# Performance work log

Measured on AMD Instinct MI355X. Metric: run time of the kernel, lower is better.

The kernel has to match this reference:

```python
import jax, jax.numpy as jnp
import numpy as np

B, S, D, H = 4, 2048, 1024, 16
HD = D // H

def setup_inputs() -> dict:
    key = jax.random.key(0)
    ks = jax.random.split(key, 10)
    s = 1.0 / np.sqrt(D)
    inp = {
        'x': jax.random.normal(ks[0], (B, S, D), dtype=jnp.float32),
        'attention_mask': jnp.ones((B, S), dtype=jnp.int32),
        'Wq': jax.random.uniform(ks[1], (D, D), jnp.float32, -s, s),
        'bq': jax.random.uniform(ks[2], (D,), jnp.float32, -s, s),
        'Wk': jax.random.uniform(ks[3], (D, D), jnp.float32, -s, s),
        'bk': jax.random.uniform(ks[4], (D,), jnp.float32, -s, s),
        'Wv': jax.random.uniform(ks[5], (D, D), jnp.float32, -s, s),
        'bv': jax.random.uniform(ks[6], (D,), jnp.float32, -s, s),
        'Wo': jax.random.uniform(ks[7], (D, D), jnp.float32, -s, s),
        'bo': jax.random.uniform(ks[8], (D,), jnp.float32, -s, s),
    }
    return inp

def reference(x, Wq, bq, Wk, bk, Wv, bv, Wo, bo, attention_mask):
    scale = HD ** -0.5
    # torch Linear: y = x @ W^T + b
    def proj(W, b):
        return (x @ W.T + b).reshape(B, S, H, HD).transpose(0, 2, 1, 3)  # [B,H,S,hd]
    q = proj(Wq, bq)
    k = proj(Wk, bk)
    v = proj(Wv, bv)
    scores = jnp.einsum('bhqd,bhkd->bhqk', q, k) * scale  # [B,H,S,S]
    causal = jnp.triu(jnp.ones((S, S), dtype=bool), k=1)
    scores = jnp.where(causal, -jnp.inf, scores)
    pad = (attention_mask == 0)[:, None, None, :]  # [B,1,1,S]
    scores = jnp.where(pad, jnp.float32(-1e9), scores)
    probs = jax.nn.softmax(scores, axis=-1)
    out = jnp.einsum('bhqk,bhkd->bhqd', probs, v)  # [B,H,S,hd]
    out = out.transpose(0, 2, 1, 3).reshape(B, S, D)
    return out @ Wo.T + bo
```

## Files before the change

kernel.cpp:

```cpp
#include <hip/hip_runtime.h>
#include <hip/hip_bf16.h>

typedef unsigned short u16;
typedef float f32x4 __attribute__((ext_vector_type(4)));
typedef __bf16 bf16x8 __attribute__((ext_vector_type(8)));

#define BB 4
#define SS 2048
#define DD 1024
#define HH 16
#define HDD 64
#define MM (BB*SS)

__device__ __forceinline__ u16 f2bf(float f){
    union { float f; unsigned int i; } v; v.f = f;
    unsigned int i = v.i;
    return (u16)((i + 0x7FFFu + ((i >> 16) & 1u)) >> 16);
}
__device__ __forceinline__ ushort2 pk2(float a, float b){
    union { __hip_bfloat162 h; ushort2 u; } v;
    float2 t; t.x = a; t.y = b;
    v.h = __float22bfloat162_rn(t);
    return v.u;
}
__device__ __forceinline__ ushort4 pk4(float a, float b, float c, float d){
    ushort2 lo = pk2(a, b), hi = pk2(c, d);
    ushort4 r; r.x = lo.x; r.y = lo.y; r.z = hi.x; r.w = hi.y;
    return r;
}
__device__ __forceinline__ void gl2lds16(const void* g, void* l){
    __builtin_amdgcn_global_load_lds(
        (const __attribute__((address_space(1))) void*)g,
        (__attribute__((address_space(3))) void*)l, 16, 0, 0);
}

__device__ __forceinline__ void cvt8(const float* __restrict__ src,
                                     u16* __restrict__ dst, size_t i)
{
    const float4 a = *(const float4*)&src[i];
    const float4 b = *(const float4*)&src[i + 4];
    ushort4 lo = pk4(a.x, a.y, a.z, a.w);
    ushort4 hi = pk4(b.x, b.y, b.z, b.w);
    uint4 o;
    o.x = (unsigned)lo.x | ((unsigned)lo.y << 16);
    o.y = (unsigned)lo.z | ((unsigned)lo.w << 16);
    o.z = (unsigned)hi.x | ((unsigned)hi.y << 16);
    o.w = (unsigned)hi.z | ((unsigned)hi.w << 16);
    *(uint4*)&dst[i] = o;
}

__global__ __launch_bounds__(256) void cvt_k(const float* __restrict__ src,
                                             u16* __restrict__ dst)
{
    const size_t i = ((size_t)blockIdx.x * 256 + threadIdx.x) * 8;
    cvt8(src, dst, i);
}

__global__ __launch_bounds__(256) void cvtw_k(
    const float* __restrict__ W0, const float* __restrict__ W1,
    const float* __restrict__ W2, const float* __restrict__ W3,
    u16* __restrict__ dst)
{
    const float* src = blockIdx.y == 0 ? W0 : (blockIdx.y == 1 ? W1 :
                        (blockIdx.y == 2 ? W2 : W3));
    u16* d = dst + (size_t)blockIdx.y * (size_t)DD * DD;
    const size_t i = ((size_t)blockIdx.x * 256 + threadIdx.x) * 8;
    cvt8(src, d, i);
}

template<bool WB>
__device__ __forceinline__ void gemm_core_t(const u16* __restrict__ A,
                                            const float* __restrict__ Wf,
                                            const u16* __restrict__ Wb,
                                            f32x4 (&acc)[4][4],
                                            u16* At, u16* Bt,
                                            int m0, int n0, int tid)
{
    const int lane = tid & 63, w = tid >> 6;
    const int quad = lane >> 4, l15 = lane & 15;
    const int wm = w >> 1, wn = w & 1;
    const int arow = lane >> 2;
    const int acol = (lane & 3) * 8;

    for (int k0 = 0; k0 < DD; k0 += 32) {
        __syncthreads();
        #pragma unroll
        for (int c = 0; c < 2; ++c) {
            const int ch = w * 2 + c;
            gl2lds16(&A[(size_t)(m0 + ch * 16 + arow) * DD + k0 + acol], &At[ch * 512]);
        }
        if (WB) {
            #pragma unroll
            for (int c = 0; c < 2; ++c) {
                const int ch = w * 2 + c;
                gl2lds16(&Wb[(size_t)(n0 + ch * 16 + arow) * DD + k0 + acol], &Bt[ch * 512]);
            }
        } else {
            #pragma unroll
            for (int it = 0; it < 2; ++it) {
                const int c = tid + it * 256;
                const int row = c >> 2, cc = (c & 3) * 8;
                const size_t woff = (size_t)(n0 + row) * DD + k0 + cc;
                const float4 u0 = *(const float4*)&Wf[woff];
                const float4 u1 = *(const float4*)&Wf[woff + 4];
                ushort4 lo = pk4(u0.x, u0.y, u0.z, u0.w);
                ushort4 hi = pk4(u1.x, u1.y, u1.z, u1.w);
                uint4 o;
                o.x = (unsigned)lo.x | ((unsigned)lo.y << 16);
                o.y = (unsigned)lo.z | ((unsigned)lo.w << 16);
                o.z = (unsigned)hi.x | ((unsigned)hi.y << 16);
                o.w = (unsigned)hi.z | ((unsigned)hi.w << 16);
                *(uint4*)&Bt[row * 32 + cc] = o;
            }
        }
        __syncthreads();
        bf16x8 af[4], bfr[4];
        #pragma unroll
        for (int i = 0; i < 4; ++i)
            af[i] = *(const bf16x8*)&At[(wm * 64 + i * 16 + l15) * 32 + quad * 8];
        #pragma unroll
        for (int j = 0; j < 4; ++j)
            bfr[j] = *(const bf16x8*)&Bt[(wn * 64 + j * 16 + l15) * 32 + quad * 8];
        #pragma unroll
        for (int i = 0; i < 4; ++i)
            #pragma unroll
            for (int j = 0; j < 4; ++j)
                acc[i][j] = __builtin_amdgcn_mfma_f32_16x16x32_bf16(af[i], bfr[j], acc[i][j], 0, 0, 0);
    }
}

template<bool WB>
__global__ __launch_bounds__(256, 4) void gemm_qkv_k(
    const u16* __restrict__ x,
    const float* __restrict__ Wq, const float* __restrict__ bq,
    const float* __restrict__ Wk, const float* __restrict__ bk,
    const float* __restrict__ Wv, const float* __restrict__ bv,
    const u16* __restrict__ Wqb, const u16* __restrict__ Wkb,
    const u16* __restrict__ Wvb,
    u16* __restrict__ Q, u16* __restrict__ K, u16* __restrict__ V)
{
    __shared__ alignas(16) u16 At[128 * 32];
    __shared__ alignas(16) u16 Bt[128 * 32];
    const int tid = threadIdx.x, lane = tid & 63, w = tid >> 6;
    const int quad = lane >> 4, l15 = lane & 15;
    const int wm = w >> 1, wn = w & 1;
    const int z = blockIdx.z;
    const float* Wm = z == 0 ? Wq : (z == 1 ? Wk : Wv);
    const u16* Wmb = z == 0 ? Wqb : (z == 1 ? Wkb : Wvb);
    const float* bias = z == 0 ? bq : (z == 1 ? bk : bv);
    u16* Out = z == 0 ? Q : (z == 1 ? K : V);
    const int m0 = blockIdx.x * 128, n0 = blockIdx.y * 128;

    f32x4 acc[4][4];
    #pragma unroll
    for (int i = 0; i < 4; ++i)
        #pragma unroll
        for (int j = 0; j < 4; ++j) acc[i][j] = (f32x4)(0.0f);

    gemm_core_t<WB>(x, Wm, Wmb, acc, At, Bt, m0, n0, tid);

    float bs[4];
    #pragma unroll
    for (int j = 0; j < 4; ++j) bs[j] = bias[n0 + wn * 64 + j * 16 + l15];

    const int b = m0 / SS;
    const int h = (n0 + wn * 64) / HDD;
    const size_t base = ((size_t)(b * HH + h)) * SS * HDD;
    #pragma unroll
    for (int i = 0; i < 4; ++i) {
        #pragma unroll
        for (int r = 0; r < 4; ++r) {
            const int s = (m0 % SS) + wm * 64 + i * 16 + quad * 4 + r;
            #pragma unroll
            for (int j = 0; j < 4; ++j) {
                const int hd = j * 16 + l15;
                Out[base + (size_t)s * HDD + hd] = f2bf(acc[i][j][r] + bs[j]);
            }
        }
    }
}

template<bool WB>
__global__ __launch_bounds__(256, 4) void gemm_out_k(
    const u16* __restrict__ A, const float* __restrict__ Wo,
    const float* __restrict__ bo, const u16* __restrict__ Wob,
    float* __restrict__ Out)
{
    __shared__ alignas(16) u16 At[128 * 32];
    __shared__ alignas(16) u16 Bt[128 * 32];
    const int tid = threadIdx.x, lane = tid & 63, w = tid >> 6;
    const int quad = lane >> 4, l15 = lane & 15;
    const int wm = w >> 1, wn = w & 1;
    const int m0 = blockIdx.x * 128, n0 = blockIdx.y * 128;

    f32x4 acc[4][4];
    #pragma unroll
    for (int i = 0; i < 4; ++i)
        #pragma unroll
        for (int j = 0; j < 4; ++j) acc[i][j] = (f32x4)(0.0f);

    gemm_core_t<WB>(A, Wo, Wob, acc, At, Bt, m0, n0, tid);

    float bs[4];
    #pragma unroll
    for (int j = 0; j < 4; ++j) bs[j] = bo[n0 + wn * 64 + j * 16 + l15];

    #pragma unroll
    for (int i = 0; i < 4; ++i) {
        #pragma unroll
        for (int r = 0; r < 4; ++r) {
            const int m = m0 + wm * 64 + i * 16 + quad * 4 + r;
            #pragma unroll
            for (int j = 0; j < 4; ++j) {
                const int n = n0 + wn * 64 + j * 16 + l15;
                Out[(size_t)m * DD + n] = acc[i][j][r] + bs[j];
            }
        }
    }
}

#define QT 256
#define KT 64
#define LDP 72
#define LDPV 66

#define LOG2E 1.4426950408889634f

__global__ __launch_bounds__(512, 2) void attn_k(
    const u16* __restrict__ Q, const u16* __restrict__ K,
    const u16* __restrict__ V, const int* __restrict__ mask,
    u16* __restrict__ AO)
{
    __shared__ alignas(16) u16 QPs[QT * LDP];
    __shared__ alignas(16) u16 Ks[2][KT * LDP];
    __shared__ alignas(16) u16 Vs[2][HDD * LDPV];
    __shared__ alignas(16) float padf[2][KT];

    const int tid = threadIdx.x, lane = tid & 63, w = tid >> 6;
    const int quad = lane >> 4, l15 = lane & 15;
    const int bh = blockIdx.x;
    const int y = blockIdx.y;
    const int qt = (y < 4) ? (7 - y) : (y - 4);
    const int b = bh >> 4, h = bh & 15;
    const int q0 = qt * QT;
    const size_t hoff = (size_t)bh * SS * HDD;
    const u16* Qh = Q + hoff;
    const u16* Kh = K + hoff;
    const u16* Vh = V + hoff;
    const int nkt = (q0 + QT) / KT;
    const float scale2 = 0.125f * LOG2E;

    uint4 kr0, kr1, vr0, vr1, vr2, vr3;
    float pr = 0.f;

    auto LOADT = [&](int kt0) {
        if (tid < 256) {
            const int row0 = tid >> 3, cc0 = (tid & 7) * 8;
            kr0 = *(const uint4*)&Kh[(size_t)(kt0 + row0) * HDD + cc0];
            const int row1 = (tid + 256) >> 3, cc1 = ((tid + 256) & 7) * 8;
            kr1 = *(const uint4*)&Kh[(size_t)(kt0 + row1) * HDD + cc1];
        } else if (tid < 384) {
            const int t = tid - 256;
            const int kq = t >> 3, c0 = (t & 7) * 8;
            vr0 = *(const uint4*)&Vh[(size_t)(kt0 + kq * 4 + 0) * HDD + c0];
            vr1 = *(const uint4*)&Vh[(size_t)(kt0 + kq * 4 + 1) * HDD + c0];
            vr2 = *(const uint4*)&Vh[(size_t)(kt0 + kq * 4 + 2) * HDD + c0];
            vr3 = *(const uint4*)&Vh[(size_t)(kt0 + kq * 4 + 3) * HDD + c0];
        } else if (tid < 448) {
            pr = (mask[b * SS + kt0 + (tid - 384)] == 0) ? -1e9f : 0.0f;
        }
    };
    auto WRITET = [&](int bb) {
        if (tid < 256) {
            const int row0 = tid >> 3, cc0 = (tid & 7) * 8;
            *(uint4*)&Ks[bb][row0 * LDP + cc0] = kr0;
            const int row1 = (tid + 256) >> 3, cc1 = ((tid + 256) & 7) * 8;
            *(uint4*)&Ks[bb][row1 * LDP + cc1] = kr1;
        } else if (tid < 384) {
            const int t = tid - 256;
            const int kq = t >> 3, c0 = (t & 7) * 8;
            const u16* e0 = (const u16*)&vr0;
            const u16* e1 = (const u16*)&vr1;
            const u16* e2 = (const u16*)&vr2;
            const u16* e3 = (const u16*)&vr3;
            #pragma unroll
            for (int e = 0; e < 8; ++e) {
                ushort4 pkv; pkv.x = e0[e]; pkv.y = e1[e]; pkv.z = e2[e]; pkv.w = e3[e];
                *(ushort4*)&Vs[bb][(c0 + e) * LDPV + kq * 4] = pkv;
            }
        } else if (tid < 448) {
            padf[bb][tid - 384] = pr;
        }
    };

    LOADT(0);

    for (int c = tid; c < QT * 8; c += 512) {
        const int row = c >> 3, cc = c & 7;
        *(uint4*)&QPs[row * LDP + cc * 8] = *(const uint4*)&Qh[(size_t)(q0 + row) * HDD + cc * 8];
    }
    WRITET(0);
    __syncthreads();

    bf16x8 bQ[2][2];
    #pragma unroll
    for (int j = 0; j < 2; ++j)
        #pragma unroll
        for (int ks = 0; ks < 2; ++ks)
            bQ[j][ks] = *(const bf16x8*)&QPs[(w * 32 + j * 16 + l15) * LDP + ks * 32 + quad * 8];

    float m_run[2] = { -1e30f, -1e30f };
    float l_run[2] = { 0.f, 0.f };
    f32x4 o[4][2];
    #pragma unroll
    for (int i = 0; i < 4; ++i)
        #pragma unroll
        for (int j = 0; j < 2; ++j) o[i][j] = (f32x4)(0.0f);

    for (int kt = 0; kt < nkt; ++kt) {
        const int cur = kt & 1;
        const int kt0 = kt * KT;
        if (kt + 1 < nkt) LOADT(kt0 + KT);

        const u16* KsC = Ks[cur];
        const u16* VsC = Vs[cur];
        const float* padfC = padf[cur];

        f32x4 sc[4][2];
        #pragma unroll
        for (int i = 0; i < 4; ++i)
            #pragma unroll
            for (int j = 0; j < 2; ++j) sc[i][j] = (f32x4)(0.0f);
        __builtin_amdgcn_s_setprio(1);
        #pragma unroll
        for (int ks = 0; ks < 2; ++ks) {
            bf16x8 aK[4];
            #pragma unroll
            for (int i = 0; i < 4; ++i)
                aK[i] = *(const bf16x8*)&KsC[(i * 16 + l15) * LDP + ks * 32 + quad * 8];
            #pragma unroll
            for (int i = 0; i < 4; ++i)
                #pragma unroll
                for (int j = 0; j < 2; ++j)
                    sc[i][j] = __builtin_amdgcn_mfma_f32_16x16x32_bf16(aK[i], bQ[j][ks], sc[i][j], 0, 0, 0);
        }
        __builtin_amdgcn_s_setprio(0);

        f32x4 pb[4];
        #pragma unroll
        for (int i = 0; i < 4; ++i)
            pb[i] = *(const f32x4*)&padfC[i * 16 + quad * 4];

        #pragma unroll
        for (int j = 0; j < 2; ++j) {
            const int qrow = q0 + w * 32 + j * 16 + l15;
            const bool needC = (kt0 + KT - 1) > (q0 + w * 32 + j * 16);
            float mx = -1e9f;
            if (needC) {
                #pragma unroll
                for (int i = 0; i < 4; ++i)
                    #pragma unroll
                    for (int r = 0; r < 4; ++r) {
                        const int kpg = kt0 + i * 16 + quad * 4 + r;
                        float s = fmaf(sc[i][j][r], scale2, pb[i][r]);
                        s = (kpg > qrow) ? -1e9f : s;
                        sc[i][j][r] = s; mx = fmaxf(mx, s);
                    }
            } else {
                #pragma unroll
                for (int i = 0; i < 4; ++i)
                    #pragma unroll
                    for (int r = 0; r < 4; ++r) {
                        float s = fmaf(sc[i][j][r], scale2, pb[i][r]);
                        sc[i][j][r] = s; mx = fmaxf(mx, s);
                    }
            }
            mx = fmaxf(mx, __shfl_xor(mx, 16, 64));
            mx = fmaxf(mx, __shfl_xor(mx, 32, 64));
            float nm = m_run[j];
            if (!__all(mx <= nm + 8.f)) {
                nm = fmaxf(nm, mx);
                const float alpha = __builtin_exp2f(m_run[j] - nm);
                m_run[j] = nm;
                l_run[j] *= alpha;
                #pragma unroll
                for (int i = 0; i < 4; ++i)
                    #pragma unroll
                    for (int r = 0; r < 4; ++r) o[i][j][r] *= alpha;
            }
            float rs = 0.f;
            #pragma unroll
            for (int i = 0; i < 4; ++i) {
                float p0 = __builtin_exp2f(sc[i][j][0] - nm);
                float p1 = __builtin_exp2f(sc[i][j][1] - nm);
                float p2 = __builtin_exp2f(sc[i][j][2] - nm);
                float p3 = __builtin_exp2f(sc[i][j][3] - nm);
                rs += (p0 + p1) + (p2 + p3);
                *(ushort4*)&QPs[(w * 32 + j * 16 + l15) * LDP + i * 16 + quad * 4] = pk4(p0, p1, p2, p3);
            }
            l_run[j] += rs;
        }
        asm volatile("s_waitcnt lgkmcnt(0)" ::: "memory");

        __builtin_amdgcn_s_setprio(1);
        #pragma unroll
        for (int ks = 0; ks < 2; ++ks) {
            bf16x8 aV[4], bP[2];
            #pragma unroll
            for (int i = 0; i < 4; ++i)
                aV[i] = *(const bf16x8*)&VsC[(i * 16 + l15) * LDPV + ks * 32 + quad * 8];
            #pragma unroll
            for (int j = 0; j < 2; ++j)
                bP[j] = *(const bf16x8*)&QPs[(w * 32 + j * 16 + l15) * LDP + ks * 32 + quad * 8];
            #pragma unroll
            for (int i = 0; i < 4; ++i)
                #pragma unroll
                for (int j = 0; j < 2; ++j)
                    o[i][j] = __builtin_amdgcn_mfma_f32_16x16x32_bf16(aV[i], bP[j], o[i][j], 0, 0, 0);
        }
        __builtin_amdgcn_s_setprio(0);

        if (kt + 1 < nkt) WRITET(cur ^ 1);
        __syncthreads();
    }

    #pragma unroll
    for (int j = 0; j < 2; ++j) {
        float l = l_run[j];
        l += __shfl_xor(l, 16, 64);
        l += __shfl_xor(l, 32, 64);
        const float inv = (l > 0.f) ? (1.f / l) : 0.f;
        const int s = q0 + w * 32 + j * 16 + l15;
        const size_t rb = ((size_t)(b * SS + s)) * DD + h * HDD;
        #pragma unroll
        for (int i = 0; i < 4; ++i)
            *(ushort4*)&AO[rb + i * 16 + quad * 4] =
                pk4(o[i][j][0] * inv, o[i][j][1] * inv, o[i][j][2] * inv, o[i][j][3] * inv);
    }
}

extern "C" void kernel_launch(void* const* d_in, const int* in_sizes, int n_in,
                              void* d_out, int out_size, void* d_ws, size_t ws_size,
                              hipStream_t stream)
{
    const float* x  = (const float*)d_in[0];
    const int* mask = (const int*)d_in[1];
    const float* Wq = (const float*)d_in[2];
    const float* bq = (const float*)d_in[3];
    const float* Wk = (const float*)d_in[4];
    const float* bk = (const float*)d_in[5];
    const float* Wv = (const float*)d_in[6];
    const float* bv = (const float*)d_in[7];
    const float* Wo = (const float*)d_in[8];
    const float* bo = (const float*)d_in[9];
    float* out = (float*)d_out;

    u16* ws = (u16*)d_ws;
    const size_t NE = (size_t)MM * DD;
    const size_t WE = (size_t)DD * DD;
    if (ws_size < 4 * NE * sizeof(u16)) return;
    const bool wb = ws_size >= (4 * NE + 4 * WE) * sizeof(u16);

    u16* Qb = ws;
    u16* Kb = ws + NE;
    u16* Vb = ws + 2 * NE;
    u16* Ab = ws + 3 * NE;

    dim3 blk(256);
    cvt_k<<<dim3(NE / 2048), blk, 0, stream>>>(x, Ab);
    if (wb) {
        u16* Wbase = ws + 4 * NE;
        cvtw_k<<<dim3(WE / 2048, 4), blk, 0, stream>>>(Wq, Wk, Wv, Wo, Wbase);
        gemm_qkv_k<true><<<dim3(MM / 128, DD / 128, 3), blk, 0, stream>>>(
            Ab, Wq, bq, Wk, bk, Wv, bv,
            Wbase, Wbase + WE, Wbase + 2 * WE, Qb, Kb, Vb);
        attn_k<<<dim3(BB * HH, SS / QT), dim3(512), 0, stream>>>(Qb, Kb, Vb, mask, Ab);
        gemm_out_k<true><<<dim3(MM / 128, DD / 128), blk, 0, stream>>>(
            Ab, Wo, bo, Wbase + 3 * WE, out);
    } else {
        gemm_qkv_k<false><<<dim3(MM / 128, DD / 128, 3), blk, 0, stream>>>(
            Ab, Wq, bq, Wk, bk, Wv, bv,
            nullptr, nullptr, nullptr, Qb, Kb, Vb);
        attn_k<<<dim3(BB * HH, SS / QT), dim3(512), 0, stream>>>(Qb, Kb, Vb, mask, Ab);
        gemm_out_k<false><<<dim3(MM / 128, DD / 128), blk, 0, stream>>>(
            Ab, Wo, bo, nullptr, out);
    }
}
```

Before: 359.9 us.

## Drop K/V double buffering, swizzle LDS, raise attention occupancy to 3 blocks

The attention kernel drops the register-staged double buffer for K, V and the pad mask and loads each tile directly into a single LDS buffer, with a barrier before and after each load. Q/P and K tiles switch from padded rows to an XOR-swizzled 128-byte row layout, which cuts LDS footprint and avoids bank conflicts. With less LDS and fewer live staging registers, launch bounds ask for 3 blocks per CU instead of 2. The trade-off is that global load latency is no longer overlapped within a block and must be hidden by the extra resident blocks, plus an added barrier per tile.

```diff
diff --git a/kernel.cpp b/kernel.cpp
--- a/kernel.cpp
+++ b/kernel.cpp
@@ -221,20 +221,23 @@
 
 #define QT 256
 #define KT 64
-#define LDP 72
 #define LDPV 66
 
 #define LOG2E 1.4426950408889634f
 
-__global__ __launch_bounds__(512, 2) void attn_k(
+__device__ __forceinline__ int swz128(int row, int bcol){
+    return row * 128 + (bcol ^ ((row & 7) << 4));
+}
+
+__global__ __launch_bounds__(512, 3) void attn_k(
     const u16* __restrict__ Q, const u16* __restrict__ K,
     const u16* __restrict__ V, const int* __restrict__ mask,
     u16* __restrict__ AO)
 {
-    __shared__ alignas(16) u16 QPs[QT * LDP];
-    __shared__ alignas(16) u16 Ks[2][KT * LDP];
-    __shared__ alignas(16) u16 Vs[2][HDD * LDPV];
-    __shared__ alignas(16) float padf[2][KT];
+    __shared__ alignas(16) u16 QPs[QT * 64];
+    __shared__ alignas(16) u16 Ks[KT * 64];
+    __shared__ alignas(16) u16 Vs[HDD * LDPV];
+    __shared__ float padf[KT];
 
     const int tid = threadIdx.x, lane = tid & 63, w = tid >> 6;
     const int quad = lane >> 4, l15 = lane & 15;
@@ -250,56 +253,11 @@
     const int nkt = (q0 + QT) / KT;
     const float scale2 = 0.125f * LOG2E;
 
-    uint4 kr0, kr1, vr0, vr1, vr2, vr3;
-    float pr = 0.f;
-
-    auto LOADT = [&](int kt0) {
-        if (tid < 256) {
-            const int row0 = tid >> 3, cc0 = (tid & 7) * 8;
-            kr0 = *(const uint4*)&Kh[(size_t)(kt0 + row0) * HDD + cc0];
-            const int row1 = (tid + 256) >> 3, cc1 = ((tid + 256) & 7) * 8;
-            kr1 = *(const uint4*)&Kh[(size_t)(kt0 + row1) * HDD + cc1];
-        } else if (tid < 384) {
-            const int t = tid - 256;
-            const int kq = t >> 3, c0 = (t & 7) * 8;
-            vr0 = *(const uint4*)&Vh[(size_t)(kt0 + kq * 4 + 0) * HDD + c0];
-            vr1 = *(const uint4*)&Vh[(size_t)(kt0 + kq * 4 + 1) * HDD + c0];
-            vr2 = *(const uint4*)&Vh[(size_t)(kt0 + kq * 4 + 2) * HDD + c0];
-            vr3 = *(const uint4*)&Vh[(size_t)(kt0 + kq * 4 + 3) * HDD + c0];
-        } else if (tid < 448) {
-            pr = (mask[b * SS + kt0 + (tid - 384)] == 0) ? -1e9f : 0.0f;
-        }
-    };
-    auto WRITET = [&](int bb) {
-        if (tid < 256) {
-            const int row0 = tid >> 3, cc0 = (tid & 7) * 8;
-            *(uint4*)&Ks[bb][row0 * LDP + cc0] = kr0;
-            const int row1 = (tid + 256) >> 3, cc1 = ((tid + 256) & 7) * 8;
-            *(uint4*)&Ks[bb][row1 * LDP + cc1] = kr1;
-        } else if (tid < 384) {
-            const int t = tid - 256;
-            const int kq = t >> 3, c0 = (t & 7) * 8;
-            const u16* e0 = (const u16*)&vr0;
-            const u16* e1 = (const u16*)&vr1;
-            const u16* e2 = (const u16*)&vr2;
-            const u16* e3 = (const u16*)&vr3;
-            #pragma unroll
-            for (int e = 0; e < 8; ++e) {
-                ushort4 pkv; pkv.x = e0[e]; pkv.y = e1[e]; pkv.z = e2[e]; pkv.w = e3[e];
-                *(ushort4*)&Vs[bb][(c0 + e) * LDPV + kq * 4] = pkv;
-            }
-        } else if (tid < 448) {
-            padf[bb][tid - 384] = pr;
-        }
-    };
-
-    LOADT(0);
-
     for (int c = tid; c < QT * 8; c += 512) {
         const int row = c >> 3, cc = c & 7;
-        *(uint4*)&QPs[row * LDP + cc * 8] = *(const uint4*)&Qh[(size_t)(q0 + row) * HDD + cc * 8];
-    }
-    WRITET(0);
+        *(uint4*)((char*)QPs + swz128(row, cc * 16)) =
+            *(const uint4*)&Qh[(size_t)(q0 + row) * HDD + cc * 8];
+    }
     __syncthreads();
 
     bf16x8 bQ[2][2];
@@ -307,7 +265,8 @@
     for (int j = 0; j < 2; ++j)
         #pragma unroll
         for (int ks = 0; ks < 2; ++ks)
-            bQ[j][ks] = *(const bf16x8*)&QPs[(w * 32 + j * 16 + l15) * LDP + ks * 32 + quad * 8];
+            bQ[j][ks] = *(const bf16x8*)((const char*)QPs +
+                swz128(w * 32 + j * 16 + l15, ks * 64 + quad * 16));
 
     float m_run[2] = { -1e30f, -1e30f };
     float l_run[2] = { 0.f, 0.f };
@@ -318,13 +277,39 @@
         for (int j = 0; j < 2; ++j) o[i][j] = (f32x4)(0.0f);
 
     for (int kt = 0; kt < nkt; ++kt) {
-        const int cur = kt & 1;
         const int kt0 = kt * KT;
-        if (kt + 1 < nkt) LOADT(kt0 + KT);
-
-        const u16* KsC = Ks[cur];
-        const u16* VsC = Vs[cur];
-        const float* padfC = padf[cur];
+        __syncthreads();
+
+        if (tid < 256) {
+            #pragma unroll
+            for (int it = 0; it < 2; ++it) {
+                const int c = tid + it * 256;
+                const int row = c >> 3, cc = c & 7;
+                *(uint4*)((char*)Ks + swz128(row, cc * 16)) =
+                    *(const uint4*)&Kh[(size_t)(kt0 + row) * HDD + cc * 8];
+            }
+        } else if (tid < 384) {
+            const int t = tid - 256;
+            const int kq = t >> 3;
+            const int c0 = (t & 7) * 8;
+            uint4 r0 = *(const uint4*)&Vh[(size_t)(kt0 + kq * 4 + 0) * HDD + c0];
+            uint4 r1 = *(const uint4*)&Vh[(size_t)(kt0 + kq * 4 + 1) * HDD + c0];
+            uint4 r2 = *(const uint4*)&Vh[(size_t)(kt0 + kq * 4 + 2) * HDD + c0];
+            uint4 r3 = *(const uint4*)&Vh[(size_t)(kt0 + kq * 4 + 3) * HDD + c0];
+            const u16* e0 = (const u16*)&r0;
+            const u16* e1 = (const u16*)&r1;
+            const u16* e2 = (const u16*)&r2;
+            const u16* e3 = (const u16*)&r3;
+            #pragma unroll
+            for (int e = 0; e < 8; ++e) {
+                ushort4 pkv; pkv.x = e0[e]; pkv.y = e1[e]; pkv.z = e2[e]; pkv.w = e3[e];
+                *(ushort4*)&Vs[(c0 + e) * LDPV + kq * 4] = pkv;
+            }
+        } else if (tid < 448) {
+            const int t = tid - 384;
+            padf[t] = (mask[b * SS + kt0 + t] == 0) ? -1e9f : 0.0f;
+        }
+        __syncthreads();
 
         f32x4 sc[4][2];
         #pragma unroll
@@ -337,7 +322,8 @@
             bf16x8 aK[4];
             #pragma unroll
             for (int i = 0; i < 4; ++i)
-                aK[i] = *(const bf16x8*)&KsC[(i * 16 + l15) * LDP + ks * 32 + quad * 8];
+                aK[i] = *(const bf16x8*)((const char*)Ks +
+                    swz128(i * 16 + l15, ks * 64 + quad * 16));
             #pragma unroll
             for (int i = 0; i < 4; ++i)
                 #pragma unroll
@@ -349,7 +335,7 @@
         f32x4 pb[4];
         #pragma unroll
         for (int i = 0; i < 4; ++i)
-            pb[i] = *(const f32x4*)&padfC[i * 16 + quad * 4];
+            pb[i] = *(const f32x4*)&padf[i * 16 + quad * 4];
 
         #pragma unroll
         for (int j = 0; j < 2; ++j) {
@@ -396,7 +382,8 @@
                 float p2 = __builtin_exp2f(sc[i][j][2] - nm);
                 float p3 = __builtin_exp2f(sc[i][j][3] - nm);
                 rs += (p0 + p1) + (p2 + p3);
-                *(ushort4*)&QPs[(w * 32 + j * 16 + l15) * LDP + i * 16 + quad * 4] = pk4(p0, p1, p2, p3);
+                *(ushort4*)((char*)QPs + swz128(w * 32 + j * 16 + l15, i * 32 + quad * 8)) =
+                    pk4(p0, p1, p2, p3);
             }
             l_run[j] += rs;
         }
@@ -408,10 +395,11 @@
             bf16x8 aV[4], bP[2];
             #pragma unroll
             for (int i = 0; i < 4; ++i)
-                aV[i] = *(const bf16x8*)&VsC[(i * 16 + l15) * LDPV + ks * 32 + quad * 8];
+                aV[i] = *(const bf16x8*)&Vs[(i * 16 + l15) * LDPV + ks * 32 + quad * 8];
             #pragma unroll
             for (int j = 0; j < 2; ++j)
-                bP[j] = *(const bf16x8*)&QPs[(w * 32 + j * 16 + l15) * LDP + ks * 32 + quad * 8];
+                bP[j] = *(const bf16x8*)((const char*)QPs +
+                    swz128(w * 32 + j * 16 + l15, ks * 64 + quad * 16));
             #pragma unroll
             for (int i = 0; i < 4; ++i)
                 #pragma unroll
@@ -419,9 +407,6 @@
                     o[i][j] = __builtin_amdgcn_mfma_f32_16x16x32_bf16(aV[i], bP[j], o[i][j], 0, 0, 0);
         }
         __builtin_amdgcn_s_setprio(0);
-
-        if (kt + 1 < nkt) WRITET(cur ^ 1);
-        __syncthreads();
     }
 
     #pragma unroll
```

After: 317.5 us. 11.8% less time.
